# Kernel tuning notes

Hardware: AMD Instinct MI355X
Metric: run time of the kernel (lower is better)

Reference implementation:

```python
import jax, jax.numpy as jnp
import numpy as np

NU = 0.01
RHO = 1.0
WSCALE = 0.05  # keep activations sane for deep randn-initialized MLP


def _mlp(z, Win, b_in, Wh, b_h, Wout, b_out):
    # z: (3,) -> (2,) = (psi, p)
    h = jax.nn.relu(z @ Win + b_in)
    for i in range(Wh.shape[0]):  # static, small layer loop
        h = jax.nn.relu(h @ Wh[i] + b_h[i])
    return h @ Wout + b_out


def _point(z, Win, b_in, Wh, b_h, Wout, b_out):
    # z = (x, y, t)
    psi_fn = lambda zz: _mlp(zz, Win, b_in, Wh, b_h, Wout, b_out)[0]
    p_fn = lambda zz: _mlp(zz, Win, b_in, Wh, b_h, Wout, b_out)[1]
    u_fn = lambda zz: jax.grad(psi_fn)(zz)[1]   # u = dpsi/dy
    v_fn = lambda zz: -jax.grad(psi_fn)(zz)[0]  # v = -dpsi/dx
    u = u_fn(z)
    v = v_fn(z)
    p = p_fn(z)
    gu = jax.grad(u_fn)(z)   # (u_x, u_y, u_t)
    gv = jax.grad(v_fn)(z)   # (v_x, v_y, v_t)
    gp = jax.grad(p_fn)(z)   # (p_x, p_y, p_t)
    Hu = jax.jacfwd(jax.grad(u_fn))(z)  # 3x3 Hessian of u
    Hv = jax.jacfwd(jax.grad(v_fn))(z)
    f = gu[2] + u * gu[0] + v * gu[1] + gp[0] / RHO - NU * (Hu[0, 0] + Hu[1, 1])
    g = gv[2] + u * gv[0] + v * gv[1] + gp[1] / RHO - NU * (Hv[0, 0] + Hv[1, 1])
    return u, v, p, f, g


def setup_inputs() -> dict:
    key = jax.random.key(0)
    ks = jax.random.split(key, 6)
    N, H, L = 65536, 256, 6
    x = jax.random.normal(ks[0], (N, 1), dtype=jnp.float32)
    y = jax.random.normal(ks[1], (N, 1), dtype=jnp.float32)
    t = jax.random.uniform(ks[2], (N, 1), dtype=jnp.float32)
    Win = jax.random.normal(ks[3], (3, H), dtype=jnp.float32) * WSCALE
    b_in = jnp.zeros((H,), dtype=jnp.float32)
    Wh = jax.random.normal(ks[4], (L - 2, H, H), dtype=jnp.float32) * WSCALE
    b_h = jnp.zeros((L - 2, H), dtype=jnp.float32)
    Wout = jax.random.normal(ks[5], (H, 2), dtype=jnp.float32) * WSCALE
    b_out = jnp.zeros((2,), dtype=jnp.float32)
    return {"x": x, "y": y, "t": t, "Win": Win, "b_in": b_in,
            "Wh": Wh, "b_h": b_h, "Wout": Wout, "b_out": b_out}


def reference(x, y, t, Win, b_in, Wh, b_h, Wout, b_out):
    z = jnp.concatenate([x, y, t], axis=1)  # (N, 3)
    u, v, p, f, g = jax.vmap(_point, in_axes=(0, None, None, None, None, None, None))(
        z, Win, b_in, Wh, b_h, Wout, b_out)
    col = lambda a: a[:, None]  # (N,) -> (N,1)
    return col(u), col(v), col(p), col(f), col(g)
```

## Files before the change

### kernel.cpp

```cpp
#include <hip/hip_runtime.h>
#include <hip/hip_bf16.h>


#define NPTS 65536
#define HDIM 256

typedef _Float16 half8_t __attribute__((ext_vector_type(8)));
typedef _Float16 half4_t __attribute__((ext_vector_type(4)));
typedef float floatx4 __attribute__((ext_vector_type(4)));

__global__ void __launch_bounds__(1024) fwd_fused_kernel(
    const float* __restrict__ x, const float* __restrict__ y, const float* __restrict__ t,
    const float* __restrict__ Win, const float* __restrict__ b_in,
    const float* __restrict__ Wh, const float* __restrict__ b_h,
    const float* __restrict__ Wout, const float* __restrict__ b_out,
    unsigned char* __restrict__ masks, float* __restrict__ out) {
  constexpr int SH = 257;
  __shared__ float hT[128 * SH];
  __shared__ float pscr[16][132];

  const int tid = threadIdx.x;
  const int lane = tid & 63;
  const int w = __builtin_amdgcn_readfirstlane(tid >> 6);
  const int c0 = w * 16;
  const int p0 = blockIdx.x * 128;
  const int pA = p0 + lane;
  const int pB = p0 + 64 + lane;

  {
    float xa = x[pA], ya = y[pA], ta = t[pA];
    float xb = x[pB], yb = y[pB], tb = t[pB];
    unsigned ma = 0, mb = 0;
#pragma unroll
    for (int e = 0; e < 16; ++e) {
      int c = c0 + e;
      float w0 = Win[c], w1 = Win[256 + c], w2 = Win[512 + c], bb = b_in[c];
      float da = fmaf(xa, w0, 0.f);
      da = fmaf(ya, w1, da);
      da = fmaf(ta, w2, da);
      float aa = da + bb;
      bool posa = aa > 0.f;
      hT[lane * SH + c] = posa ? aa : 0.f;
      ma |= (posa ? 1u : 0u) << e;
      float db = fmaf(xb, w0, 0.f);
      db = fmaf(yb, w1, db);
      db = fmaf(tb, w2, db);
      float ab = db + bb;
      bool posb = ab > 0.f;
      hT[(64 + lane) * SH + c] = posb ? ab : 0.f;
      mb |= (posb ? 1u : 0u) << e;
    }
    *(unsigned short*)(masks + (size_t)pA * 32 + w * 2) = (unsigned short)ma;
    *(unsigned short*)(masks + (size_t)pB * 32 + w * 2) = (unsigned short)mb;
  }
  __syncthreads();

  for (int l = 0; l < 4; ++l) {
    const float* Wl = Wh + (size_t)l * 65536 + c0;
    float accA[16] = {};
    float accB[16] = {};
#pragma unroll 2
    for (int k = 0; k < 256; ++k) {
      float hA = hT[lane * SH + k];
      float hB = hT[(64 + lane) * SH + k];
      const float* wr = Wl + k * 256;
#pragma unroll
      for (int e = 0; e < 16; ++e) {
        float wv = wr[e];
        accA[e] = fmaf(hA, wv, accA[e]);
        accB[e] = fmaf(hB, wv, accB[e]);
      }
    }
    __syncthreads();
    unsigned ma = 0, mb = 0;
    float hnA[16], hnB[16];
#pragma unroll
    for (int e = 0; e < 16; ++e) {
      float bb = b_h[l * 256 + c0 + e];
      float aa = accA[e] + bb;
      bool posa = aa > 0.f;
      hnA[e] = posa ? aa : 0.f;
      ma |= (posa ? 1u : 0u) << e;
      float ab = accB[e] + bb;
      bool posb = ab > 0.f;
      hnB[e] = posb ? ab : 0.f;
      mb |= (posb ? 1u : 0u) << e;
    }
    *(unsigned short*)(masks + ((size_t)(l + 1) * NPTS + pA) * 32 + w * 2) =
        (unsigned short)ma;
    *(unsigned short*)(masks + ((size_t)(l + 1) * NPTS + pB) * 32 + w * 2) =
        (unsigned short)mb;
#pragma unroll
    for (int e = 0; e < 16; ++e) {
      hT[lane * SH + c0 + e] = hnA[e];
      hT[(64 + lane) * SH + c0 + e] = hnB[e];
    }
    __syncthreads();
  }

  {
    float sA = 0.f, sB = 0.f;
#pragma unroll
    for (int e = 0; e < 16; ++e) {
      float wv = Wout[2 * (c0 + e) + 1];
      sA = fmaf(hT[lane * SH + c0 + e], wv, sA);
      sB = fmaf(hT[(64 + lane) * SH + c0 + e], wv, sB);
    }
    pscr[w][lane] = sA;
    pscr[w][64 + lane] = sB;
  }
  __syncthreads();
  if (tid < 128) {
    float s2 = 0.f;
#pragma unroll
    for (int g = 0; g < 16; ++g) s2 += pscr[g][tid];
    out[2 * NPTS + p0 + tid] = s2 + b_out[1];
  }
}

__global__ void __launch_bounds__(256) prep_weights_kernel(
    const float* __restrict__ Wh, _Float16* __restrict__ Wt2) {
  int i = blockIdx.x * 256 + threadIdx.x;
  int j = i & 7;
  int lane = (i >> 3) & 63;
  int nj = (i >> 9) & 3;
  int s = (i >> 11) & 7;
  int wn = (i >> 14) & 3;
  int l = i >> 16;
  int k = s * 32 + ((lane >> 4) << 3) + j;
  int n = wn * 64 + nj * 16 + (lane & 15);
  Wt2[i] = (_Float16)Wh[(size_t)l * 65536 + (size_t)k * 256 + n];
}

__global__ void __launch_bounds__(256, 2) tangent_fused_kernel(
    const float* __restrict__ Win,
    const _Float16* __restrict__ Wt2,
    const unsigned int* __restrict__ maskDw,
    const float* __restrict__ Wout, float* __restrict__ out) {
  constexpr int SA = 264;
  __shared__ alignas(16) _Float16 Apan[64 * SA];
  __shared__ unsigned int smask[5 * 256];

  const int tid = threadIdx.x;
  const int lane = tid & 63;
  const int wn = tid >> 6;
  const int l15 = lane & 15, quad = lane >> 4;
  const int p0 = blockIdx.x * 32;

#pragma unroll
  for (int i = 0; i < 5; ++i)
    smask[i * 256 + tid] = maskDw[(size_t)i * NPTS * 8 + (size_t)p0 * 8 + tid];
  __syncthreads();

#pragma unroll
  for (int i = 0; i < 8; ++i) {
    int g = tid + 256 * i;
    int row = g >> 5, cg = g & 31;
    int c0 = cg * 8, pt = row & 31, tg = row >> 5;
    unsigned dw = smask[pt * 8 + (c0 >> 5)];
    half8_t v;
#pragma unroll
    for (int e = 0; e < 8; ++e) {
      bool m = (dw >> ((cg & 3) * 8 + e)) & 1;
      v[e] = m ? (_Float16)Win[tg * 256 + c0 + e] : (_Float16)0.f;
    }
    *(half8_t*)&Apan[row * SA + c0] = v;
  }
  __syncthreads();

  for (int l = 0; l < 4; ++l) {
    const _Float16* Bw = Wt2 + ((size_t)(l * 4 + wn) * 32 + 0) * 512 + (size_t)lane * 8;

    half8_t breg[8][4];
#pragma unroll
    for (int s = 0; s < 8; ++s)
#pragma unroll
      for (int nj = 0; nj < 4; ++nj)
        breg[s][nj] = *(const half8_t*)(Bw + (size_t)(s * 4 + nj) * 512);

    floatx4 acc[4][4] = {};
#pragma unroll
    for (int s = 0; s < 8; ++s) {
      half8_t af[4];
#pragma unroll
      for (int mi = 0; mi < 4; ++mi)
        af[mi] = *(const half8_t*)&Apan[(mi * 16 + l15) * SA + s * 32 + quad * 8];
#pragma unroll
      for (int mi = 0; mi < 4; ++mi)
#pragma unroll
        for (int nj = 0; nj < 4; ++nj)
          acc[mi][nj] = __builtin_amdgcn_mfma_f32_16x16x32_f16(breg[s][nj], af[mi], acc[mi][nj], 0, 0, 0);
    }
    __syncthreads();
    const unsigned int* ml = &smask[(l + 1) * 256];
    uint2 mA = *(const uint2*)&ml[l15 * 8 + wn * 2];
    uint2 mB = *(const uint2*)&ml[(16 + l15) * 8 + wn * 2];
#pragma unroll
    for (int mi = 0; mi < 4; ++mi) {
      uint2 md = (mi & 1) ? mB : mA;
      int m = mi * 16 + l15;
#pragma unroll
      for (int nj = 0; nj < 4; ++nj) {
        unsigned dw = (nj < 2) ? md.x : md.y;
        int bitbase = (nj & 1) * 16 + quad * 4;
        half4_t v;
#pragma unroll
        for (int r = 0; r < 4; ++r)
          v[r] = ((dw >> (bitbase + r)) & 1) ? (_Float16)acc[mi][nj][r]
                                             : (_Float16)0.f;
        *(half4_t*)&Apan[m * SA + wn * 64 + nj * 16 + quad * 4] = v;
      }
    }
    __syncthreads();
  }

  {
    floatx4 facc = {0.f, 0.f, 0.f, 0.f};
#pragma unroll
    for (int kc = 0; kc < 8; ++kc) {
      half8_t a = *(const half8_t*)&Apan[(wn * 16 + l15) * SA + kc * 32 + quad * 8];
      half8_t b;
#pragma unroll
      for (int j = 0; j < 8; ++j) {
        int k = kc * 32 + quad * 8 + j;
        b[j] = (l15 < 2) ? (_Float16)Wout[2 * k + l15] : (_Float16)0.f;
      }
      facc = __builtin_amdgcn_mfma_f32_16x16x32_f16(a, b, facc, 0, 0, 0);
    }
    if (l15 < 2) {
#pragma unroll
      for (int r = 0; r < 4; ++r) {
        int row = wn * 16 + quad * 4 + r;
        int pt = p0 + (row & 31);
        float val = facc[r];
        if (l15 == 0) {
          if (row < 32) out[NPTS + pt] = -val;
          else          out[pt] = val;
        } else {
          if (row < 32) out[3 * NPTS + pt] = val;
          else          out[4 * NPTS + pt] = val;
        }
      }
    }
  }
}

extern "C" void kernel_launch(void* const* d_in, const int* in_sizes, int n_in,
                              void* d_out, int out_size, void* d_ws, size_t ws_size,
                              hipStream_t stream) {
  const float* x = (const float*)d_in[0];
  const float* y = (const float*)d_in[1];
  const float* t = (const float*)d_in[2];
  const float* Win = (const float*)d_in[3];
  const float* b_in = (const float*)d_in[4];
  const float* Wh = (const float*)d_in[5];
  const float* b_h = (const float*)d_in[6];
  const float* Wout = (const float*)d_in[7];
  const float* b_out = (const float*)d_in[8];
  float* out = (float*)d_out;

  char* ws = (char*)d_ws;
  constexpr size_t MASK_SZ = (size_t)NPTS * 32;
  unsigned char* masks = (unsigned char*)ws;
  _Float16* Wt2 = (_Float16*)(ws + 5 * MASK_SZ);

  prep_weights_kernel<<<1024, 256, 0, stream>>>(Wh, Wt2);

  fwd_fused_kernel<<<NPTS / 128, 1024, 0, stream>>>(
      x, y, t, Win, b_in, Wh, b_h, Wout, b_out, masks, out);

  tangent_fused_kernel<<<NPTS / 32, 256, 0, stream>>>(
      Win, Wt2, (const unsigned int*)masks, Wout, out);
}
```

Before: 510.9 us.

## Double tangent kernel tile to 64 points and double-buffer weight fragments

The tangent kernel now processes 64 points per block (128 tangent rows) instead of 32, so each weight fragment loaded from global memory is reused across twice as many MFMA rows. The full per-layer B register preload is replaced with a two-stage double buffer that loads the next k-slice while the current one is computed. In exchange the accumulators double (8x4 floatx4), LDS use roughly doubles, and there are half as many blocks, which may lower occupancy and push register pressure toward spilling.

```diff
diff --git a/kernel.cpp b/kernel.cpp
--- a/kernel.cpp
+++ b/kernel.cpp
@@ -138,25 +138,28 @@
     const unsigned int* __restrict__ maskDw,
     const float* __restrict__ Wout, float* __restrict__ out) {
   constexpr int SA = 264;
-  __shared__ alignas(16) _Float16 Apan[64 * SA];
-  __shared__ unsigned int smask[5 * 256];
+  __shared__ alignas(16) _Float16 Apan[128 * SA];
+  __shared__ unsigned int smask[5 * 512];
 
   const int tid = threadIdx.x;
   const int lane = tid & 63;
   const int wn = tid >> 6;
   const int l15 = lane & 15, quad = lane >> 4;
-  const int p0 = blockIdx.x * 32;
-
-#pragma unroll
-  for (int i = 0; i < 5; ++i)
-    smask[i * 256 + tid] = maskDw[(size_t)i * NPTS * 8 + (size_t)p0 * 8 + tid];
-  __syncthreads();
-
-#pragma unroll
-  for (int i = 0; i < 8; ++i) {
+  const int p0 = blockIdx.x * 64;
+
+#pragma unroll
+  for (int i = 0; i < 10; ++i) {
+    int idx = i * 256 + tid;
+    int layer = idx >> 9, rem = idx & 511;
+    smask[idx] = maskDw[(size_t)layer * NPTS * 8 + (size_t)p0 * 8 + rem];
+  }
+  __syncthreads();
+
+#pragma unroll
+  for (int i = 0; i < 16; ++i) {
     int g = tid + 256 * i;
     int row = g >> 5, cg = g & 31;
-    int c0 = cg * 8, pt = row & 31, tg = row >> 5;
+    int c0 = cg * 8, pt = row & 63, tg = row >> 6;
     unsigned dw = smask[pt * 8 + (c0 >> 5)];
     half8_t v;
 #pragma unroll
@@ -169,35 +172,41 @@
   __syncthreads();
 
   for (int l = 0; l < 4; ++l) {
-    const _Float16* Bw = Wt2 + ((size_t)(l * 4 + wn) * 32 + 0) * 512 + (size_t)lane * 8;
-
-    half8_t breg[8][4];
-#pragma unroll
-    for (int s = 0; s < 8; ++s)
-#pragma unroll
-      for (int nj = 0; nj < 4; ++nj)
-        breg[s][nj] = *(const half8_t*)(Bw + (size_t)(s * 4 + nj) * 512);
-
-    floatx4 acc[4][4] = {};
+    const _Float16* Bw = Wt2 + (size_t)(l * 4 + wn) * 32 * 512 + (size_t)lane * 8;
+
+    floatx4 acc[8][4] = {};
+    half8_t bb[2][4];
+#pragma unroll
+    for (int nj = 0; nj < 4; ++nj)
+      bb[0][nj] = *(const half8_t*)(Bw + (size_t)(0 * 4 + nj) * 512);
+
 #pragma unroll
     for (int s = 0; s < 8; ++s) {
-      half8_t af[4];
-#pragma unroll
-      for (int mi = 0; mi < 4; ++mi)
+      if (s < 7) {
+#pragma unroll
+        for (int nj = 0; nj < 4; ++nj)
+          bb[(s + 1) & 1][nj] =
+              *(const half8_t*)(Bw + (size_t)((s + 1) * 4 + nj) * 512);
+      }
+      half8_t af[8];
+#pragma unroll
+      for (int mi = 0; mi < 8; ++mi)
         af[mi] = *(const half8_t*)&Apan[(mi * 16 + l15) * SA + s * 32 + quad * 8];
 #pragma unroll
-      for (int mi = 0; mi < 4; ++mi)
+      for (int mi = 0; mi < 8; ++mi)
 #pragma unroll
         for (int nj = 0; nj < 4; ++nj)
-          acc[mi][nj] = __builtin_amdgcn_mfma_f32_16x16x32_f16(breg[s][nj], af[mi], acc[mi][nj], 0, 0, 0);
-    }
-    __syncthreads();
-    const unsigned int* ml = &smask[(l + 1) * 256];
-    uint2 mA = *(const uint2*)&ml[l15 * 8 + wn * 2];
-    uint2 mB = *(const uint2*)&ml[(16 + l15) * 8 + wn * 2];
-#pragma unroll
-    for (int mi = 0; mi < 4; ++mi) {
-      uint2 md = (mi & 1) ? mB : mA;
+          acc[mi][nj] = __builtin_amdgcn_mfma_f32_16x16x32_f16(bb[s & 1][nj], af[mi], acc[mi][nj], 0, 0, 0);
+    }
+    __syncthreads();
+    const unsigned int* ml = &smask[(l + 1) * 512];
+    uint2 mPT[4];
+#pragma unroll
+    for (int q = 0; q < 4; ++q)
+      mPT[q] = *(const uint2*)&ml[(q * 16 + l15) * 8 + wn * 2];
+#pragma unroll
+    for (int mi = 0; mi < 8; ++mi) {
+      uint2 md = mPT[mi & 3];
       int m = mi * 16 + l15;
 #pragma unroll
       for (int nj = 0; nj < 4; ++nj) {
@@ -215,30 +224,37 @@
   }
 
   {
-    floatx4 facc = {0.f, 0.f, 0.f, 0.f};
+    floatx4 f0 = {0.f, 0.f, 0.f, 0.f};
+    floatx4 f1 = {0.f, 0.f, 0.f, 0.f};
 #pragma unroll
     for (int kc = 0; kc < 8; ++kc) {
-      half8_t a = *(const half8_t*)&Apan[(wn * 16 + l15) * SA + kc * 32 + quad * 8];
+      half8_t a0 = *(const half8_t*)&Apan[(wn * 32 + l15) * SA + kc * 32 + quad * 8];
+      half8_t a1 = *(const half8_t*)&Apan[(wn * 32 + 16 + l15) * SA + kc * 32 + quad * 8];
       half8_t b;
 #pragma unroll
       for (int j = 0; j < 8; ++j) {
         int k = kc * 32 + quad * 8 + j;
         b[j] = (l15 < 2) ? (_Float16)Wout[2 * k + l15] : (_Float16)0.f;
       }
-      facc = __builtin_amdgcn_mfma_f32_16x16x32_f16(a, b, facc, 0, 0, 0);
+      f0 = __builtin_amdgcn_mfma_f32_16x16x32_f16(a0, b, f0, 0, 0, 0);
+      f1 = __builtin_amdgcn_mfma_f32_16x16x32_f16(a1, b, f1, 0, 0, 0);
     }
     if (l15 < 2) {
 #pragma unroll
-      for (int r = 0; r < 4; ++r) {
-        int row = wn * 16 + quad * 4 + r;
-        int pt = p0 + (row & 31);
-        float val = facc[r];
-        if (l15 == 0) {
-          if (row < 32) out[NPTS + pt] = -val;
-          else          out[pt] = val;
-        } else {
-          if (row < 32) out[3 * NPTS + pt] = val;
-          else          out[4 * NPTS + pt] = val;
+      for (int c = 0; c < 2; ++c) {
+        floatx4 fc = c ? f1 : f0;
+#pragma unroll
+        for (int r = 0; r < 4; ++r) {
+          int row = wn * 32 + c * 16 + quad * 4 + r;
+          int pt = p0 + (row & 63);
+          float val = fc[r];
+          if (l15 == 0) {
+            if (row < 64) out[NPTS + pt] = -val;
+            else          out[pt] = val;
+          } else {
+            if (row < 64) out[3 * NPTS + pt] = val;
+            else          out[4 * NPTS + pt] = val;
+          }
         }
       }
     }
@@ -269,6 +285,6 @@
   fwd_fused_kernel<<<NPTS / 128, 1024, 0, stream>>>(
       x, y, t, Win, b_in, Wh, b_h, Wout, b_out, masks, out);
 
-  tangent_fused_kernel<<<NPTS / 32, 256, 0, stream>>>(
+  tangent_fused_kernel<<<NPTS / 64, 256, 0, stream>>>(
       Win, Wt2, (const unsigned int*)masks, Wout, out);
 }
```

Result: no change. 520.9 us (+2.0%).
